# Performance work log

Hardware: AMD Instinct MI355X
Metric: run time of the kernel (lower is better)

The kernel has to match this reference:

```python
import jax, jax.numpy as jnp
import numpy as np

B, S, D = 2, 2048, 2048
H, KVH, HD = 32, 8, 64
ROPE_THETA = 500000.0


def _rope_cos_sin(seq_len, head_dim, theta, batch):
    inv_freq = 1.0 / (theta ** (jnp.arange(0, head_dim, 2, dtype=jnp.float32) / head_dim))  # [HD/2]
    pos = jnp.arange(seq_len, dtype=jnp.float32)
    freqs = jnp.outer(pos, inv_freq)                      # [S, HD/2]
    emb = jnp.concatenate([freqs, freqs], axis=-1)        # [S, HD]
    cos = jnp.broadcast_to(jnp.cos(emb), (batch, seq_len, head_dim))
    sin = jnp.broadcast_to(jnp.sin(emb), (batch, seq_len, head_dim))
    return cos, sin


def setup_inputs() -> dict:
    key = jax.random.key(0)
    kx, kq, kk, kv, ko = jax.random.split(key, 5)
    x = jax.random.normal(kx, (B, S, D), dtype=jnp.float32)
    cos, sin = _rope_cos_sin(S, HD, ROPE_THETA, B)
    scale = 0.02
    Wq = jax.random.normal(kq, (H * HD, D), dtype=jnp.float32) * scale
    Wk = jax.random.normal(kk, (KVH * HD, D), dtype=jnp.float32) * scale
    Wv = jax.random.normal(kv, (KVH * HD, D), dtype=jnp.float32) * scale
    Wo = jax.random.normal(ko, (D, H * HD), dtype=jnp.float32) * scale
    return {"x": x, "cos": cos, "sin": sin, "Wq": Wq, "Wk": Wk, "Wv": Wv, "Wo": Wo}


def rotate_half(t):
    t1, t2 = jnp.split(t, 2, axis=-1)
    return jnp.concatenate([-t2, t1], axis=-1)


def reference(x, cos, sin, Wq, Wk, Wv, Wo):
    b, s, d = x.shape
    scaling = HD ** -0.5
    groups = H // KVH
    # projections (torch Linear: y = x @ W.T)
    q = jnp.einsum('bsd,od->bso', x, Wq).reshape(b, s, H, HD).transpose(0, 2, 1, 3)    # [B,H,S,HD]
    k = jnp.einsum('bsd,od->bso', x, Wk).reshape(b, s, KVH, HD).transpose(0, 2, 1, 3)  # [B,KVH,S,HD]
    v = jnp.einsum('bsd,od->bso', x, Wv).reshape(b, s, KVH, HD).transpose(0, 2, 1, 3)
    # RoPE (cos/sin unsqueezed over head dim)
    c = cos[:, None, :, :]
    sn = sin[:, None, :, :]
    q = q * c + rotate_half(q) * sn
    k = k * c + rotate_half(k) * sn
    # GQA: repeat kv heads
    k = jnp.repeat(k, groups, axis=1)  # [B,H,S,HD]
    v = jnp.repeat(v, groups, axis=1)
    # causal eager SDPA
    scores = jnp.einsum('bhqd,bhkd->bhqk', q, k) * scaling
    causal = jnp.tril(jnp.ones((s, s), dtype=bool))
    scores = jnp.where(causal[None, None], scores, jnp.finfo(scores.dtype).min)
    attn_weights = jax.nn.softmax(scores, axis=-1)
    attn = jnp.einsum('bhqk,bhkd->bhqd', attn_weights, v)
    attn = attn.transpose(0, 2, 1, 3).reshape(b, s, H * HD)
    out = jnp.einsum('bso,do->bsd', attn, Wo)
    return out
```

## Files before the change

### kernel.cpp

```cpp
#include <hip/hip_runtime.h>
#include <hip/hip_bf16.h>

typedef __attribute__((ext_vector_type(8))) short bf16x8_t;
typedef __attribute__((ext_vector_type(4))) float f32x4;

#define S_LEN  2048
#define NB     2
#define NH     32
#define NKVH   8
#define HD     64
#define DMODEL 2048
#define SCALE  0.125f
#define CEXP   0.18033688f
#define THRRAW 44.0f

__device__ __forceinline__ void gload16(const __hip_bfloat16* g, __hip_bfloat16* l) {
  __builtin_amdgcn_global_load_lds(
      (const __attribute__((address_space(1))) void*)g,
      (__attribute__((address_space(3))) void*)l, 16, 0, 0);
}

struct CvtSeg { const float* src; __hip_bfloat16* dst; int n4; };
struct CvtArgs { CvtSeg s[5]; };

__global__ __launch_bounds__(256) void cvt_all(CvtArgs a) {
  int i = blockIdx.x * blockDim.x + threadIdx.x;
#pragma unroll
  for (int k = 0; k < 5; ++k) {
    if (i < a.s[k].n4) {
      float4 v = ((const float4*)a.s[k].src)[i];
      __hip_bfloat16 o0 = __float2bfloat16(v.x), o1 = __float2bfloat16(v.y);
      __hip_bfloat16 o2 = __float2bfloat16(v.z), o3 = __float2bfloat16(v.w);
      ushort4 pk;
      pk.x = *(unsigned short*)&o0; pk.y = *(unsigned short*)&o1;
      pk.z = *(unsigned short*)&o2; pk.w = *(unsigned short*)&o3;
      ((ushort4*)a.s[k].dst)[i] = pk;
      return;
    }
    i -= a.s[k].n4;
  }
}

__global__ __launch_bounds__(256)
void gemm_qkv(const __hip_bfloat16* __restrict__ A,
              const __hip_bfloat16* __restrict__ Wq,
              const __hip_bfloat16* __restrict__ Wk,
              const __hip_bfloat16* __restrict__ Wv,
              __hip_bfloat16* __restrict__ Qo,
              __hip_bfloat16* __restrict__ Ko,
              __hip_bfloat16* __restrict__ Vto,
              const float* __restrict__ cosb,
              const float* __restrict__ sinb)
{
  __shared__ __align__(16) __hip_bfloat16 As[2][128][32];
  __shared__ __align__(16) __hip_bfloat16 Bs[2][128][32];
  const int K = DMODEL;

  const int tid  = threadIdx.x;
  const int lane = tid & 63;
  const int w    = tid >> 6;
  const int wr   = (w >> 1) * 64;
  const int wc   = (w & 1) * 64;
  const int brow = blockIdx.y * 128;
  const int fr   = lane & 15;
  const int fg   = lane >> 4;

  const int bc = blockIdx.x * 128;
  const __hip_bfloat16* Bt; int bcol; int path;
  if (bc < 2048)      { Bt = Wq; bcol = bc;        path = 0; }
  else if (bc < 2560) { Bt = Wk; bcol = bc - 2048; path = 1; }
  else                { Bt = Wv; bcol = bc - 2560; path = 2; }

  const f32x4 fz = {0.f, 0.f, 0.f, 0.f};
  f32x4 acc[4][4];
#pragma unroll
  for (int i = 0; i < 4; ++i)
#pragma unroll
    for (int j = 0; j < 4; ++j) acc[i][j] = fz;

  const int lrow = lane >> 2;
  const int lcol = (lane & 3) * 8;
  const __hip_bfloat16* Ag = A  + (size_t)(brow + w * 32 + lrow) * K + lcol;
  const __hip_bfloat16* Bg = Bt + (size_t)(bcol + w * 32 + lrow) * K + lcol;

  auto stage = [&](int buf, int kt) {
    gload16(Ag + kt,                    &As[buf][w * 32][0]);
    gload16(Ag + (size_t)16 * K + kt,   &As[buf][w * 32 + 16][0]);
    gload16(Bg + kt,                    &Bs[buf][w * 32][0]);
    gload16(Bg + (size_t)16 * K + kt,   &Bs[buf][w * 32 + 16][0]);
  };

  stage(0, 0);
  __syncthreads();
  int cur = 0;
  for (int kt = 0; kt < K; kt += 32) {
    if (kt + 32 < K) stage(cur ^ 1, kt + 32);

    bf16x8_t af[4], bfr[4];
#pragma unroll
    for (int mi = 0; mi < 4; ++mi)
      af[mi] = *(const bf16x8_t*)&As[cur][wr + mi * 16 + fr][fg * 8];
#pragma unroll
    for (int ni = 0; ni < 4; ++ni)
      bfr[ni] = *(const bf16x8_t*)&Bs[cur][wc + ni * 16 + fr][fg * 8];
#pragma unroll
    for (int mi = 0; mi < 4; ++mi)
#pragma unroll
      for (int ni = 0; ni < 4; ++ni)
        acc[mi][ni] = __builtin_amdgcn_mfma_f32_16x16x32_bf16(af[mi], bfr[ni], acc[mi][ni], 0, 0, 0);

    __syncthreads();
    cur ^= 1;
  }

  if (path == 2) {
#pragma unroll
    for (int mi = 0; mi < 4; ++mi) {
#pragma unroll
      for (int ni = 0; ni < 4; ++ni) {
        const int row0 = brow + wr + mi * 16 + fg * 4;
        const int col  = bcol + wc + ni * 16 + fr;
        const int b = row0 >> 11, s = row0 & 2047;
        const int kvh = col >> 6, d = col & 63;
        __hip_bfloat16 v0 = __float2bfloat16(acc[mi][ni][0]);
        __hip_bfloat16 v1 = __float2bfloat16(acc[mi][ni][1]);
        __hip_bfloat16 v2 = __float2bfloat16(acc[mi][ni][2]);
        __hip_bfloat16 v3 = __float2bfloat16(acc[mi][ni][3]);
        ushort4 pk;
        pk.x = *(unsigned short*)&v0; pk.y = *(unsigned short*)&v1;
        pk.z = *(unsigned short*)&v2; pk.w = *(unsigned short*)&v3;
        *(ushort4*)&Vto[(((size_t)b * NKVH + kvh) * HD + d) * S_LEN + s] = pk;
      }
    }
  } else {
    __hip_bfloat16* C = (path == 0) ? Qo : Ko;
    const int N = (path == 0) ? (NH * HD) : (NKVH * HD);
#pragma unroll
    for (int mi = 0; mi < 4; ++mi) {
#pragma unroll
      for (int r = 0; r < 4; ++r) {
        const int row = brow + wr + mi * 16 + fg * 4 + r;
#pragma unroll
        for (int ni = 0; ni < 2; ++ni) {
          const int colL = bcol + wc + ni * 16 + fr;
          const int d    = (colL & 63);
          const float c  = cosb[(size_t)row * HD + d];
          const float sn = sinb[(size_t)row * HD + d];
          const float v0 = acc[mi][ni][r];
          const float v1 = acc[mi][ni + 2][r];
          C[(size_t)row * N + colL]      = __float2bfloat16(v0 * c - v1 * sn);
          C[(size_t)row * N + colL + 32] = __float2bfloat16(v1 * c + v0 * sn);
        }
      }
    }
  }
}

__global__ __launch_bounds__(256)
void gemm_o(const __hip_bfloat16* __restrict__ A,
            const __hip_bfloat16* __restrict__ Bt,
            float* __restrict__ C)
{
  __shared__ __align__(16) __hip_bfloat16 As[2][128][32];
  __shared__ __align__(16) __hip_bfloat16 Bs[2][128][32];
  const int K = DMODEL, N = DMODEL;

  const int tid  = threadIdx.x;
  const int lane = tid & 63;
  const int w    = tid >> 6;
  const int wr   = (w >> 1) * 64;
  const int wc   = (w & 1) * 64;
  const int brow = blockIdx.y * 128;
  const int bcol = blockIdx.x * 128;
  const int fr   = lane & 15;
  const int fg   = lane >> 4;

  const f32x4 fz = {0.f, 0.f, 0.f, 0.f};
  f32x4 acc[4][4];
#pragma unroll
  for (int i = 0; i < 4; ++i)
#pragma unroll
    for (int j = 0; j < 4; ++j) acc[i][j] = fz;

  const int lrow = lane >> 2;
  const int lcol = (lane & 3) * 8;
  const __hip_bfloat16* Ag = A  + (size_t)(brow + w * 32 + lrow) * K + lcol;
  const __hip_bfloat16* Bg = Bt + (size_t)(bcol + w * 32 + lrow) * K + lcol;

  auto stage = [&](int buf, int kt) {
    gload16(Ag + kt,                  &As[buf][w * 32][0]);
    gload16(Ag + (size_t)16 * K + kt, &As[buf][w * 32 + 16][0]);
    gload16(Bg + kt,                  &Bs[buf][w * 32][0]);
    gload16(Bg + (size_t)16 * K + kt, &Bs[buf][w * 32 + 16][0]);
  };

  stage(0, 0);
  __syncthreads();
  int cur = 0;
  for (int kt = 0; kt < K; kt += 32) {
    if (kt + 32 < K) stage(cur ^ 1, kt + 32);

    bf16x8_t af[4], bfr[4];
#pragma unroll
    for (int mi = 0; mi < 4; ++mi)
      af[mi] = *(const bf16x8_t*)&As[cur][wr + mi * 16 + fr][fg * 8];
#pragma unroll
    for (int ni = 0; ni < 4; ++ni)
      bfr[ni] = *(const bf16x8_t*)&Bs[cur][wc + ni * 16 + fr][fg * 8];
#pragma unroll
    for (int mi = 0; mi < 4; ++mi)
#pragma unroll
      for (int ni = 0; ni < 4; ++ni)
        acc[mi][ni] = __builtin_amdgcn_mfma_f32_16x16x32_bf16(af[mi], bfr[ni], acc[mi][ni], 0, 0, 0);

    __syncthreads();
    cur ^= 1;
  }

#pragma unroll
  for (int mi = 0; mi < 4; ++mi)
#pragma unroll
    for (int ni = 0; ni < 4; ++ni) {
      const int row0 = brow + wr + mi * 16 + fg * 4;
      const int col  = bcol + wc + ni * 16 + fr;
#pragma unroll
      for (int r = 0; r < 4; ++r)
        C[(size_t)(row0 + r) * N + col] = acc[mi][ni][r];
    }
}

__global__ __launch_bounds__(512, 6)
void attn_kernel(const __hip_bfloat16* __restrict__ Q, const __hip_bfloat16* __restrict__ K,
                 const __hip_bfloat16* __restrict__ Vt, __hip_bfloat16* __restrict__ O)
{
  __shared__ __align__(16) __hip_bfloat16 Ks[2][64][64];
  __shared__ __align__(16) __hip_bfloat16 Vs[2][64][64];
  __shared__ __align__(16) __hip_bfloat16 Ps[8][16][72];

  const int lane = threadIdx.x & 63;
  const int w    = threadIdx.x >> 6;
  const int fr   = lane & 15;
  const int fg   = lane >> 4;
  const int r8   = lane >> 3;
  const int j8   = lane & 7;
  const int bh   = blockIdx.y;
  const int b    = bh >> 5;
  const int h    = bh & 31;
  const int kvh  = h >> 2;
  const int qt    = gridDim.x - 1 - blockIdx.x;
  const int qbase = qt * 128;
  const int base_s = qbase + w * 16;

  const __hip_bfloat16* Qg = Q + ((size_t)(b * S_LEN + qbase)) * DMODEL + h * HD;
  const __hip_bfloat16* Kg = K + (size_t)b * S_LEN * (NKVH * HD) + kvh * HD;
  const __hip_bfloat16* Vg = Vt + ((size_t)(b * NKVH + kvh)) * HD * S_LEN;

  bf16x8_t qf[2];
#pragma unroll
  for (int kk = 0; kk < 2; ++kk)
    qf[kk] = *(const bf16x8_t*)(Qg + (size_t)(w * 16 + fr) * DMODEL + kk * 32 + fg * 8);

  const f32x4 fz = {0.f, 0.f, 0.f, 0.f};
  f32x4 acc[4];
#pragma unroll
  for (int i = 0; i < 4; ++i) acc[i] = fz;
  float m_ = -1e30f;
  float l_ = 0.f;

  auto stage = [&](int buf, int kt) {
    const int rb = (w & 3) * 16;
    if (w < 4) {
      gload16(Kg + (size_t)(kt + rb + r8)     * (NKVH * HD) + (j8 ^ r8) * 8, &Ks[buf][rb][0]);
      gload16(Kg + (size_t)(kt + rb + 8 + r8) * (NKVH * HD) + (j8 ^ r8) * 8, &Ks[buf][rb + 8][0]);
    } else {
      gload16(Vg + (size_t)(rb + r8)     * S_LEN + kt + (j8 ^ r8) * 8, &Vs[buf][rb][0]);
      gload16(Vg + (size_t)(rb + 8 + r8) * S_LEN + kt + (j8 ^ r8) * 8, &Vs[buf][rb + 8][0]);
    }
  };
  auto ldK = [&](int buf, int row, int cidx) -> bf16x8_t {
    return *(const bf16x8_t*)&Ks[buf][row][(cidx ^ (row & 7)) * 8];
  };
  auto ldV = [&](int buf, int row, int cidx) -> bf16x8_t {
    return *(const bf16x8_t*)&Vs[buf][row][(cidx ^ (row & 7)) * 8];
  };

  stage(0, 0);
  __syncthreads();
  int cur = 0;
  const int NT = 2 * qt + 2;
  for (int t = 0; t < NT; ++t) {
    const int kt = t * 64;
    if (t + 1 < NT) stage(cur ^ 1, kt + 64);

    if (kt <= base_s + 15) {
      f32x4 sc[4];
#pragma unroll
      for (int c = 0; c < 4; ++c) {
        const int krow = c * 16 + fr;
        bf16x8_t k0 = ldK(cur, krow, fg);
        bf16x8_t k1 = ldK(cur, krow, 4 + fg);
        sc[c] = __builtin_amdgcn_mfma_f32_16x16x32_bf16(k0, qf[0], fz, 0, 0, 0);
        sc[c] = __builtin_amdgcn_mfma_f32_16x16x32_bf16(k1, qf[1], sc[c], 0, 0, 0);
      }

      float p[4][4];
      float tm = -3.0e38f;
      if (kt + 63 > base_s) {
#pragma unroll
        for (int c = 0; c < 4; ++c)
#pragma unroll
          for (int r = 0; r < 4; ++r) {
            float v = sc[c][r];
            if (kt + c * 16 + fg * 4 + r > base_s + fr) v = -3.0e38f;
            p[c][r] = v; tm = fmaxf(tm, v);
          }
      } else {
#pragma unroll
        for (int c = 0; c < 4; ++c)
#pragma unroll
          for (int r = 0; r < 4; ++r) { p[c][r] = sc[c][r]; tm = fmaxf(tm, sc[c][r]); }
      }
      tm = fmaxf(tm, __shfl_xor(tm, 16));
      tm = fmaxf(tm, __shfl_xor(tm, 32));

      if (!__all(tm <= m_ + THRRAW)) {
        const float mnew = fmaxf(m_, tm);
        const float sf = exp2f((m_ - mnew) * CEXP);
        m_ = mnew;
        l_ *= sf;
        float sfv[4];
#pragma unroll
        for (int r = 0; r < 4; ++r) sfv[r] = __shfl(sf, fg * 4 + r);
#pragma unroll
        for (int fc = 0; fc < 4; ++fc)
#pragma unroll
          for (int r = 0; r < 4; ++r) acc[fc][r] *= sfv[r];
      }

      float ts = 0.f;
#pragma unroll
      for (int c = 0; c < 4; ++c)
#pragma unroll
        for (int r = 0; r < 4; ++r) {
          p[c][r] = exp2f((p[c][r] - m_) * CEXP);
          ts += p[c][r];
        }
      l_ += ts;

#pragma unroll
      for (int c = 0; c < 4; ++c) {
        __hip_bfloat16 b0 = __float2bfloat16(p[c][0]);
        __hip_bfloat16 b1 = __float2bfloat16(p[c][1]);
        __hip_bfloat16 b2 = __float2bfloat16(p[c][2]);
        __hip_bfloat16 b3 = __float2bfloat16(p[c][3]);
        ushort4 pk;
        pk.x = *(unsigned short*)&b0; pk.y = *(unsigned short*)&b1;
        pk.z = *(unsigned short*)&b2; pk.w = *(unsigned short*)&b3;
        *(ushort4*)&Ps[w][fr][c * 16 + fg * 4] = pk;
      }

#pragma unroll
      for (int kk = 0; kk < 2; ++kk) {
        bf16x8_t pa = *(const bf16x8_t*)&Ps[w][fr][kk * 32 + fg * 8];
#pragma unroll
        for (int fc = 0; fc < 4; ++fc) {
          bf16x8_t vf = ldV(cur, fc * 16 + fr, kk * 4 + fg);
          acc[fc] = __builtin_amdgcn_mfma_f32_16x16x32_bf16(pa, vf, acc[fc], 0, 0, 0);
        }
      }
    }

    __syncthreads();
    cur ^= 1;
  }

  l_ += __shfl_xor(l_, 16);
  l_ += __shfl_xor(l_, 32);
  float lv[4];
#pragma unroll
  for (int r = 0; r < 4; ++r) lv[r] = __builtin_amdgcn_rcpf(__shfl(l_, fg * 4 + r));
#pragma unroll
  for (int fc = 0; fc < 4; ++fc)
#pragma unroll
    for (int r = 0; r < 4; ++r) {
      const size_t row = (size_t)(b * S_LEN + base_s + fg * 4 + r);
      O[row * DMODEL + h * HD + fc * 16 + fr] = __float2bfloat16(acc[fc][r] * lv[r]);
    }
}

extern "C" void kernel_launch(void* const* d_in, const int* in_sizes, int n_in,
                              void* d_out, int out_size, void* d_ws, size_t ws_size,
                              hipStream_t stream)
{
  const float* x    = (const float*)d_in[0];
  const float* cosb = (const float*)d_in[1];
  const float* sinb = (const float*)d_in[2];
  const float* Wq   = (const float*)d_in[3];
  const float* Wk   = (const float*)d_in[4];
  const float* Wv   = (const float*)d_in[5];
  const float* Wo   = (const float*)d_in[6];
  float* out = (float*)d_out;

  char* p = (char*)d_ws;
  __hip_bfloat16* x_bf    = (__hip_bfloat16*)p; p += (size_t)NB * S_LEN * DMODEL * 2;
  __hip_bfloat16* Wq_bf   = (__hip_bfloat16*)p; p += (size_t)NH * HD * DMODEL * 2;
  __hip_bfloat16* Wk_bf   = (__hip_bfloat16*)p; p += (size_t)NKVH * HD * DMODEL * 2;
  __hip_bfloat16* Wv_bf   = (__hip_bfloat16*)p; p += (size_t)NKVH * HD * DMODEL * 2;
  __hip_bfloat16* Wo_bf   = (__hip_bfloat16*)p; p += (size_t)DMODEL * NH * HD * 2;
  __hip_bfloat16* Q_bf    = (__hip_bfloat16*)p; p += (size_t)NB * S_LEN * NH * HD * 2;
  __hip_bfloat16* K_bf    = (__hip_bfloat16*)p; p += (size_t)NB * S_LEN * NKVH * HD * 2;
  __hip_bfloat16* Vt_bf   = (__hip_bfloat16*)p; p += (size_t)NB * NKVH * HD * S_LEN * 2;
  __hip_bfloat16* attn_bf = (__hip_bfloat16*)p; p += (size_t)NB * S_LEN * NH * HD * 2;

  CvtArgs ca;
  ca.s[0] = { x,  x_bf,  (int)((size_t)NB * S_LEN * DMODEL / 4) };
  ca.s[1] = { Wq, Wq_bf, (int)((size_t)NH * HD * DMODEL / 4) };
  ca.s[2] = { Wk, Wk_bf, (int)((size_t)NKVH * HD * DMODEL / 4) };
  ca.s[3] = { Wv, Wv_bf, (int)((size_t)NKVH * HD * DMODEL / 4) };
  ca.s[4] = { Wo, Wo_bf, (int)((size_t)DMODEL * NH * HD / 4) };
  int total4 = ca.s[0].n4 + ca.s[1].n4 + ca.s[2].n4 + ca.s[3].n4 + ca.s[4].n4;
  cvt_all<<<(total4 + 255) / 256, 256, 0, stream>>>(ca);

  gemm_qkv<<<dim3(3072 / 128, (NB * S_LEN) / 128), dim3(256), 0, stream>>>(
      x_bf, Wq_bf, Wk_bf, Wv_bf, Q_bf, K_bf, Vt_bf, cosb, sinb);

  attn_kernel<<<dim3(S_LEN / 128, NB * NH), dim3(512), 0, stream>>>(Q_bf, K_bf, Vt_bf, attn_bf);

  gemm_o<<<dim3(DMODEL / 128, (NB * S_LEN) / 128), dim3(256), 0, stream>>>(attn_bf, Wo_bf, out);
}
```

Before: 377.3 us.

## Load attention K/V directly from global per wave and swizzle blocks across XCDs

The attention kernel drops the shared-memory double-buffered K/V staging and block-wide barriers. Each wave now loads its K and V fragments straight from global memory into registers and runs only the key tiles its causal range needs. All three kernels also remap block IDs so neighbouring tiles are spread across the XCDs, aiming for better L2 reuse. The attention occupancy hint drops from 6 to 4 because of the extra registers. This removes LDS traffic and syncs, but the eight waves of a block now each reload the same K/V tiles from global memory/L2, and there is no software prefetch.

```diff
diff --git a/kernel.cpp b/kernel.cpp
--- a/kernel.cpp
+++ b/kernel.cpp
@@ -18,6 +18,10 @@
   __builtin_amdgcn_global_load_lds(
       (const __attribute__((address_space(1))) void*)g,
       (__attribute__((address_space(3))) void*)l, 16, 0, 0);
+}
+
+__device__ __forceinline__ int xcd_swz(int bid, int nwg) {
+  return (bid & 7) * (nwg >> 3) + (bid >> 3);
 }
 
 struct CvtSeg { const float* src; __hip_bfloat16* dst; int n4; };
@@ -61,11 +65,16 @@
   const int w    = tid >> 6;
   const int wr   = (w >> 1) * 64;
   const int wc   = (w & 1) * 64;
-  const int brow = blockIdx.y * 128;
   const int fr   = lane & 15;
   const int fg   = lane >> 4;
 
-  const int bc = blockIdx.x * 128;
+  const int nwg = gridDim.x * gridDim.y;
+  const int swz = xcd_swz(blockIdx.y * gridDim.x + blockIdx.x, nwg);
+  const int bx  = swz % gridDim.x;
+  const int by  = swz / gridDim.x;
+  const int brow = by * 128;
+
+  const int bc = bx * 128;
   const __hip_bfloat16* Bt; int bcol; int path;
   if (bc < 2048)      { Bt = Wq; bcol = bc;        path = 0; }
   else if (bc < 2560) { Bt = Wk; bcol = bc - 2048; path = 1; }
@@ -170,10 +179,15 @@
   const int w    = tid >> 6;
   const int wr   = (w >> 1) * 64;
   const int wc   = (w & 1) * 64;
-  const int brow = blockIdx.y * 128;
-  const int bcol = blockIdx.x * 128;
   const int fr   = lane & 15;
   const int fg   = lane >> 4;
+
+  const int nwg = gridDim.x * gridDim.y;
+  const int swz = xcd_swz(blockIdx.y * gridDim.x + blockIdx.x, nwg);
+  const int bx  = swz % gridDim.x;
+  const int by  = swz / gridDim.x;
+  const int brow = by * 128;
+  const int bcol = bx * 128;
 
   const f32x4 fz = {0.f, 0.f, 0.f, 0.f};
   f32x4 acc[4][4];
@@ -229,30 +243,31 @@
     }
 }
 
-__global__ __launch_bounds__(512, 6)
+__global__ __launch_bounds__(512, 4)
 void attn_kernel(const __hip_bfloat16* __restrict__ Q, const __hip_bfloat16* __restrict__ K,
                  const __hip_bfloat16* __restrict__ Vt, __hip_bfloat16* __restrict__ O)
 {
-  __shared__ __align__(16) __hip_bfloat16 Ks[2][64][64];
-  __shared__ __align__(16) __hip_bfloat16 Vs[2][64][64];
   __shared__ __align__(16) __hip_bfloat16 Ps[8][16][72];
 
   const int lane = threadIdx.x & 63;
   const int w    = threadIdx.x >> 6;
   const int fr   = lane & 15;
   const int fg   = lane >> 4;
-  const int r8   = lane >> 3;
-  const int j8   = lane & 7;
-  const int bh   = blockIdx.y;
+
+  const int nwg = gridDim.x * gridDim.y;
+  const int swz = xcd_swz(blockIdx.y * gridDim.x + blockIdx.x, nwg);
+  const int bx  = swz & 15;
+  const int bh  = swz >> 4;
   const int b    = bh >> 5;
   const int h    = bh & 31;
   const int kvh  = h >> 2;
-  const int qt    = gridDim.x - 1 - blockIdx.x;
-  const int qbase = qt * 128;
+  const int qt     = 15 - bx;
+  const int qbase  = qt * 128;
   const int base_s = qbase + w * 16;
+  const int KSTR   = NKVH * HD;
 
   const __hip_bfloat16* Qg = Q + ((size_t)(b * S_LEN + qbase)) * DMODEL + h * HD;
-  const __hip_bfloat16* Kg = K + (size_t)b * S_LEN * (NKVH * HD) + kvh * HD;
+  const __hip_bfloat16* Kg = K + (size_t)b * S_LEN * KSTR + kvh * HD;
   const __hip_bfloat16* Vg = Vt + ((size_t)(b * NKVH + kvh)) * HD * S_LEN;
 
   bf16x8_t qf[2];
@@ -267,111 +282,98 @@
   float m_ = -1e30f;
   float l_ = 0.f;
 
-  auto stage = [&](int buf, int kt) {
-    const int rb = (w & 3) * 16;
-    if (w < 4) {
-      gload16(Kg + (size_t)(kt + rb + r8)     * (NKVH * HD) + (j8 ^ r8) * 8, &Ks[buf][rb][0]);
-      gload16(Kg + (size_t)(kt + rb + 8 + r8) * (NKVH * HD) + (j8 ^ r8) * 8, &Ks[buf][rb + 8][0]);
+  const int NTw = ((base_s + 15) >> 6) + 1;
+  for (int t = 0; t < NTw; ++t) {
+    const int kt = t * 64;
+
+    const __hip_bfloat16* Kt = Kg + (size_t)(kt + fr) * KSTR + fg * 8;
+    bf16x8_t k0[4], k1[4];
+#pragma unroll
+    for (int c = 0; c < 4; ++c) {
+      k0[c] = *(const bf16x8_t*)(Kt + (size_t)(c * 16) * KSTR);
+      k1[c] = *(const bf16x8_t*)(Kt + (size_t)(c * 16) * KSTR + 32);
+    }
+
+    f32x4 sc[4];
+#pragma unroll
+    for (int c = 0; c < 4; ++c) {
+      sc[c] = __builtin_amdgcn_mfma_f32_16x16x32_bf16(k0[c], qf[0], fz, 0, 0, 0);
+      sc[c] = __builtin_amdgcn_mfma_f32_16x16x32_bf16(k1[c], qf[1], sc[c], 0, 0, 0);
+    }
+
+    const __hip_bfloat16* Vp = Vg + (size_t)fr * S_LEN + kt + fg * 8;
+    bf16x8_t v0[4], v1[4];
+#pragma unroll
+    for (int fc = 0; fc < 4; ++fc) {
+      v0[fc] = *(const bf16x8_t*)(Vp + (size_t)(fc * 16) * S_LEN);
+      v1[fc] = *(const bf16x8_t*)(Vp + (size_t)(fc * 16) * S_LEN + 32);
+    }
+
+    float p[4][4];
+    float tm = -3.0e38f;
+    if (kt + 63 > base_s) {
+#pragma unroll
+      for (int c = 0; c < 4; ++c)
+#pragma unroll
+        for (int r = 0; r < 4; ++r) {
+          float v = sc[c][r];
+          if (kt + c * 16 + fg * 4 + r > base_s + fr) v = -3.0e38f;
+          p[c][r] = v; tm = fmaxf(tm, v);
+        }
     } else {
-      gload16(Vg + (size_t)(rb + r8)     * S_LEN + kt + (j8 ^ r8) * 8, &Vs[buf][rb][0]);
-      gload16(Vg + (size_t)(rb + 8 + r8) * S_LEN + kt + (j8 ^ r8) * 8, &Vs[buf][rb + 8][0]);
-    }
-  };
-  auto ldK = [&](int buf, int row, int cidx) -> bf16x8_t {
-    return *(const bf16x8_t*)&Ks[buf][row][(cidx ^ (row & 7)) * 8];
-  };
-  auto ldV = [&](int buf, int row, int cidx) -> bf16x8_t {
-    return *(const bf16x8_t*)&Vs[buf][row][(cidx ^ (row & 7)) * 8];
-  };
-
-  stage(0, 0);
-  __syncthreads();
-  int cur = 0;
-  const int NT = 2 * qt + 2;
-  for (int t = 0; t < NT; ++t) {
-    const int kt = t * 64;
-    if (t + 1 < NT) stage(cur ^ 1, kt + 64);
-
-    if (kt <= base_s + 15) {
-      f32x4 sc[4];
-#pragma unroll
-      for (int c = 0; c < 4; ++c) {
-        const int krow = c * 16 + fr;
-        bf16x8_t k0 = ldK(cur, krow, fg);
-        bf16x8_t k1 = ldK(cur, krow, 4 + fg);
-        sc[c] = __builtin_amdgcn_mfma_f32_16x16x32_bf16(k0, qf[0], fz, 0, 0, 0);
-        sc[c] = __builtin_amdgcn_mfma_f32_16x16x32_bf16(k1, qf[1], sc[c], 0, 0, 0);
+#pragma unroll
+      for (int c = 0; c < 4; ++c)
+#pragma unroll
+        for (int r = 0; r < 4; ++r) { p[c][r] = sc[c][r]; tm = fmaxf(tm, sc[c][r]); }
+    }
+    tm = fmaxf(tm, __shfl_xor(tm, 16));
+    tm = fmaxf(tm, __shfl_xor(tm, 32));
+
+    if (!__all(tm <= m_ + THRRAW)) {
+      const float mnew = fmaxf(m_, tm);
+      const float sf = exp2f((m_ - mnew) * CEXP);
+      m_ = mnew;
+      l_ *= sf;
+      float sfv[4];
+#pragma unroll
+      for (int r = 0; r < 4; ++r) sfv[r] = __shfl(sf, fg * 4 + r);
+#pragma unroll
+      for (int fc = 0; fc < 4; ++fc)
+#pragma unroll
+        for (int r = 0; r < 4; ++r) acc[fc][r] *= sfv[r];
+    }
+
+    float ts = 0.f;
+#pragma unroll
+    for (int c = 0; c < 4; ++c)
+#pragma unroll
+      for (int r = 0; r < 4; ++r) {
+        p[c][r] = exp2f((p[c][r] - m_) * CEXP);
+        ts += p[c][r];
       }
-
-      float p[4][4];
-      float tm = -3.0e38f;
-      if (kt + 63 > base_s) {
-#pragma unroll
-        for (int c = 0; c < 4; ++c)
-#pragma unroll
-          for (int r = 0; r < 4; ++r) {
-            float v = sc[c][r];
-            if (kt + c * 16 + fg * 4 + r > base_s + fr) v = -3.0e38f;
-            p[c][r] = v; tm = fmaxf(tm, v);
-          }
-      } else {
-#pragma unroll
-        for (int c = 0; c < 4; ++c)
-#pragma unroll
-          for (int r = 0; r < 4; ++r) { p[c][r] = sc[c][r]; tm = fmaxf(tm, sc[c][r]); }
+    l_ += ts;
+
+#pragma unroll
+    for (int c = 0; c < 4; ++c) {
+      __hip_bfloat16 b0 = __float2bfloat16(p[c][0]);
+      __hip_bfloat16 b1 = __float2bfloat16(p[c][1]);
+      __hip_bfloat16 b2 = __float2bfloat16(p[c][2]);
+      __hip_bfloat16 b3 = __float2bfloat16(p[c][3]);
+      ushort4 pk;
+      pk.x = *(unsigned short*)&b0; pk.y = *(unsigned short*)&b1;
+      pk.z = *(unsigned short*)&b2; pk.w = *(unsigned short*)&b3;
+      *(ushort4*)&Ps[w][fr][c * 16 + fg * 4] = pk;
+    }
+
+#pragma unroll
+    for (int kk = 0; kk < 2; ++kk) {
+      bf16x8_t pa = *(const bf16x8_t*)&Ps[w][fr][kk * 32 + fg * 8];
+#pragma unroll
+      for (int fc = 0; fc < 4; ++fc) {
+        bf16x8_t vf = (kk == 0) ? v0[fc] : v1[fc];
+        acc[fc] = __builtin_amdgcn_mfma_f32_16x16x32_bf16(pa, vf, acc[fc], 0, 0, 0);
       }
-      tm = fmaxf(tm, __shfl_xor(tm, 16));
-      tm = fmaxf(tm, __shfl_xor(tm, 32));
-
-      if (!__all(tm <= m_ + THRRAW)) {
-        const float mnew = fmaxf(m_, tm);
-        const float sf = exp2f((m_ - mnew) * CEXP);
-        m_ = mnew;
-        l_ *= sf;
-        float sfv[4];
-#pragma unroll
-        for (int r = 0; r < 4; ++r) sfv[r] = __shfl(sf, fg * 4 + r);
-#pragma unroll
-        for (int fc = 0; fc < 4; ++fc)
-#pragma unroll
-          for (int r = 0; r < 4; ++r) acc[fc][r] *= sfv[r];
-      }
-
-      float ts = 0.f;
-#pragma unroll
-      for (int c = 0; c < 4; ++c)
-#pragma unroll
-        for (int r = 0; r < 4; ++r) {
-          p[c][r] = exp2f((p[c][r] - m_) * CEXP);
-          ts += p[c][r];
-        }
-      l_ += ts;
-
-#pragma unroll
-      for (int c = 0; c < 4; ++c) {
-        __hip_bfloat16 b0 = __float2bfloat16(p[c][0]);
-        __hip_bfloat16 b1 = __float2bfloat16(p[c][1]);
-        __hip_bfloat16 b2 = __float2bfloat16(p[c][2]);
-        __hip_bfloat16 b3 = __float2bfloat16(p[c][3]);
-        ushort4 pk;
-        pk.x = *(unsigned short*)&b0; pk.y = *(unsigned short*)&b1;
-        pk.z = *(unsigned short*)&b2; pk.w = *(unsigned short*)&b3;
-        *(ushort4*)&Ps[w][fr][c * 16 + fg * 4] = pk;
-      }
-
-#pragma unroll
-      for (int kk = 0; kk < 2; ++kk) {
-        bf16x8_t pa = *(const bf16x8_t*)&Ps[w][fr][kk * 32 + fg * 8];
-#pragma unroll
-        for (int fc = 0; fc < 4; ++fc) {
-          bf16x8_t vf = ldV(cur, fc * 16 + fr, kk * 4 + fg);
-          acc[fc] = __builtin_amdgcn_mfma_f32_16x16x32_bf16(pa, vf, acc[fc], 0, 0, 0);
-        }
-      }
-    }
-
-    __syncthreads();
-    cur ^= 1;
+    }
   }
 
   l_ += __shfl_xor(l_, 16);
```

Result: slower. 607.4 us (+61.0%).

## Double attention Q tile per block and add XCD-aware block swizzle to GEMMs

Applied to the files above, without the earlier changes.

The attention kernel now gives each wave two 16-row query subtiles, so a block covers 256 query rows. Every K/V tile staged in LDS therefore serves twice as many queries, which halves K/V global traffic and the number of blocks. The cost is more accumulator registers, so launch bounds drop occupancy from 6 to 4, and the coarser causal tiles give less load balance across blocks. Both GEMMs also remap block IDs with an XCD swizzle so that neighbouring tiles share L2.

```diff
diff --git a/kernel.cpp b/kernel.cpp
--- a/kernel.cpp
+++ b/kernel.cpp
@@ -18,6 +18,10 @@
   __builtin_amdgcn_global_load_lds(
       (const __attribute__((address_space(1))) void*)g,
       (__attribute__((address_space(3))) void*)l, 16, 0, 0);
+}
+
+__device__ __forceinline__ int xcd_swz(int bid, int nwg) {
+  return (bid & 7) * (nwg >> 3) + (bid >> 3);
 }
 
 struct CvtSeg { const float* src; __hip_bfloat16* dst; int n4; };
@@ -61,11 +65,16 @@
   const int w    = tid >> 6;
   const int wr   = (w >> 1) * 64;
   const int wc   = (w & 1) * 64;
-  const int brow = blockIdx.y * 128;
   const int fr   = lane & 15;
   const int fg   = lane >> 4;
 
-  const int bc = blockIdx.x * 128;
+  const int nwg = gridDim.x * gridDim.y;
+  const int swz = xcd_swz(blockIdx.y * gridDim.x + blockIdx.x, nwg);
+  const int bx  = swz % gridDim.x;
+  const int by  = swz / gridDim.x;
+  const int brow = by * 128;
+
+  const int bc = bx * 128;
   const __hip_bfloat16* Bt; int bcol; int path;
   if (bc < 2048)      { Bt = Wq; bcol = bc;        path = 0; }
   else if (bc < 2560) { Bt = Wk; bcol = bc - 2048; path = 1; }
@@ -170,10 +179,15 @@
   const int w    = tid >> 6;
   const int wr   = (w >> 1) * 64;
   const int wc   = (w & 1) * 64;
-  const int brow = blockIdx.y * 128;
-  const int bcol = blockIdx.x * 128;
   const int fr   = lane & 15;
   const int fg   = lane >> 4;
+
+  const int nwg = gridDim.x * gridDim.y;
+  const int swz = xcd_swz(blockIdx.y * gridDim.x + blockIdx.x, nwg);
+  const int bx  = swz % gridDim.x;
+  const int by  = swz / gridDim.x;
+  const int brow = by * 128;
+  const int bcol = bx * 128;
 
   const f32x4 fz = {0.f, 0.f, 0.f, 0.f};
   f32x4 acc[4][4];
@@ -229,7 +243,7 @@
     }
 }
 
-__global__ __launch_bounds__(512, 6)
+__global__ __launch_bounds__(512, 4)
 void attn_kernel(const __hip_bfloat16* __restrict__ Q, const __hip_bfloat16* __restrict__ K,
                  const __hip_bfloat16* __restrict__ Vt, __hip_bfloat16* __restrict__ O)
 {
@@ -248,24 +262,28 @@
   const int h    = bh & 31;
   const int kvh  = h >> 2;
   const int qt    = gridDim.x - 1 - blockIdx.x;
-  const int qbase = qt * 128;
-  const int base_s = qbase + w * 16;
+  const int qbase = qt * 256;
+  const int wbase = qbase + w * 32;
 
   const __hip_bfloat16* Qg = Q + ((size_t)(b * S_LEN + qbase)) * DMODEL + h * HD;
   const __hip_bfloat16* Kg = K + (size_t)b * S_LEN * (NKVH * HD) + kvh * HD;
   const __hip_bfloat16* Vg = Vt + ((size_t)(b * NKVH + kvh)) * HD * S_LEN;
 
-  bf16x8_t qf[2];
-#pragma unroll
-  for (int kk = 0; kk < 2; ++kk)
-    qf[kk] = *(const bf16x8_t*)(Qg + (size_t)(w * 16 + fr) * DMODEL + kk * 32 + fg * 8);
+  bf16x8_t qf[2][2];
+#pragma unroll
+  for (int s = 0; s < 2; ++s)
+#pragma unroll
+    for (int kk = 0; kk < 2; ++kk)
+      qf[s][kk] = *(const bf16x8_t*)(Qg + (size_t)(w * 32 + s * 16 + fr) * DMODEL + kk * 32 + fg * 8);
 
   const f32x4 fz = {0.f, 0.f, 0.f, 0.f};
-  f32x4 acc[4];
-#pragma unroll
-  for (int i = 0; i < 4; ++i) acc[i] = fz;
-  float m_ = -1e30f;
-  float l_ = 0.f;
+  f32x4 acc[2][4];
+#pragma unroll
+  for (int s = 0; s < 2; ++s)
+#pragma unroll
+    for (int i = 0; i < 4; ++i) acc[s][i] = fz;
+  float m_[2] = {-1e30f, -1e30f};
+  float l_[2] = {0.f, 0.f};
 
   auto stage = [&](int buf, int kt) {
     const int rb = (w & 3) * 16;
@@ -287,85 +305,90 @@
   stage(0, 0);
   __syncthreads();
   int cur = 0;
-  const int NT = 2 * qt + 2;
+  const int NT = 4 * qt + 4;
   for (int t = 0; t < NT; ++t) {
     const int kt = t * 64;
     if (t + 1 < NT) stage(cur ^ 1, kt + 64);
 
-    if (kt <= base_s + 15) {
-      f32x4 sc[4];
-#pragma unroll
-      for (int c = 0; c < 4; ++c) {
-        const int krow = c * 16 + fr;
-        bf16x8_t k0 = ldK(cur, krow, fg);
-        bf16x8_t k1 = ldK(cur, krow, 4 + fg);
-        sc[c] = __builtin_amdgcn_mfma_f32_16x16x32_bf16(k0, qf[0], fz, 0, 0, 0);
-        sc[c] = __builtin_amdgcn_mfma_f32_16x16x32_bf16(k1, qf[1], sc[c], 0, 0, 0);
-      }
-
-      float p[4][4];
-      float tm = -3.0e38f;
-      if (kt + 63 > base_s) {
+    if (kt <= wbase) {
+#pragma unroll
+      for (int s = 0; s < 2; ++s) {
+        const int base_s = wbase + s * 16;
+
+        f32x4 sc[4];
+#pragma unroll
+        for (int c = 0; c < 4; ++c) {
+          const int krow = c * 16 + fr;
+          bf16x8_t k0 = ldK(cur, krow, fg);
+          bf16x8_t k1 = ldK(cur, krow, 4 + fg);
+          sc[c] = __builtin_amdgcn_mfma_f32_16x16x32_bf16(k0, qf[s][0], fz, 0, 0, 0);
+          sc[c] = __builtin_amdgcn_mfma_f32_16x16x32_bf16(k1, qf[s][1], sc[c], 0, 0, 0);
+        }
+
+        float p[4][4];
+        float tm = -3.0e38f;
+        if (kt + 63 > base_s) {
+#pragma unroll
+          for (int c = 0; c < 4; ++c)
+#pragma unroll
+            for (int r = 0; r < 4; ++r) {
+              float v = sc[c][r];
+              if (kt + c * 16 + fg * 4 + r > base_s + fr) v = -3.0e38f;
+              p[c][r] = v; tm = fmaxf(tm, v);
+            }
+        } else {
+#pragma unroll
+          for (int c = 0; c < 4; ++c)
+#pragma unroll
+            for (int r = 0; r < 4; ++r) { p[c][r] = sc[c][r]; tm = fmaxf(tm, sc[c][r]); }
+        }
+        tm = fmaxf(tm, __shfl_xor(tm, 16));
+        tm = fmaxf(tm, __shfl_xor(tm, 32));
+
+        if (!__all(tm <= m_[s] + THRRAW)) {
+          const float mnew = fmaxf(m_[s], tm);
+          const float sf = exp2f((m_[s] - mnew) * CEXP);
+          m_[s] = mnew;
+          l_[s] *= sf;
+          float sfv[4];
+#pragma unroll
+          for (int r = 0; r < 4; ++r) sfv[r] = __shfl(sf, fg * 4 + r);
+#pragma unroll
+          for (int fc = 0; fc < 4; ++fc)
+#pragma unroll
+            for (int r = 0; r < 4; ++r) acc[s][fc][r] *= sfv[r];
+        }
+
+        float ts = 0.f;
 #pragma unroll
         for (int c = 0; c < 4; ++c)
 #pragma unroll
           for (int r = 0; r < 4; ++r) {
-            float v = sc[c][r];
-            if (kt + c * 16 + fg * 4 + r > base_s + fr) v = -3.0e38f;
-            p[c][r] = v; tm = fmaxf(tm, v);
+            p[c][r] = exp2f((p[c][r] - m_[s]) * CEXP);
+            ts += p[c][r];
           }
-      } else {
-#pragma unroll
-        for (int c = 0; c < 4; ++c)
-#pragma unroll
-          for (int r = 0; r < 4; ++r) { p[c][r] = sc[c][r]; tm = fmaxf(tm, sc[c][r]); }
-      }
-      tm = fmaxf(tm, __shfl_xor(tm, 16));
-      tm = fmaxf(tm, __shfl_xor(tm, 32));
-
-      if (!__all(tm <= m_ + THRRAW)) {
-        const float mnew = fmaxf(m_, tm);
-        const float sf = exp2f((m_ - mnew) * CEXP);
-        m_ = mnew;
-        l_ *= sf;
-        float sfv[4];
-#pragma unroll
-        for (int r = 0; r < 4; ++r) sfv[r] = __shfl(sf, fg * 4 + r);
-#pragma unroll
-        for (int fc = 0; fc < 4; ++fc)
-#pragma unroll
-          for (int r = 0; r < 4; ++r) acc[fc][r] *= sfv[r];
-      }
-
-      float ts = 0.f;
-#pragma unroll
-      for (int c = 0; c < 4; ++c)
-#pragma unroll
-        for (int r = 0; r < 4; ++r) {
-          p[c][r] = exp2f((p[c][r] - m_) * CEXP);
-          ts += p[c][r];
-        }
-      l_ += ts;
-
-#pragma unroll
-      for (int c = 0; c < 4; ++c) {
-        __hip_bfloat16 b0 = __float2bfloat16(p[c][0]);
-        __hip_bfloat16 b1 = __float2bfloat16(p[c][1]);
-        __hip_bfloat16 b2 = __float2bfloat16(p[c][2]);
-        __hip_bfloat16 b3 = __float2bfloat16(p[c][3]);
-        ushort4 pk;
-        pk.x = *(unsigned short*)&b0; pk.y = *(unsigned short*)&b1;
-        pk.z = *(unsigned short*)&b2; pk.w = *(unsigned short*)&b3;
-        *(ushort4*)&Ps[w][fr][c * 16 + fg * 4] = pk;
-      }
-
-#pragma unroll
-      for (int kk = 0; kk < 2; ++kk) {
-        bf16x8_t pa = *(const bf16x8_t*)&Ps[w][fr][kk * 32 + fg * 8];
-#pragma unroll
-        for (int fc = 0; fc < 4; ++fc) {
-          bf16x8_t vf = ldV(cur, fc * 16 + fr, kk * 4 + fg);
-          acc[fc] = __builtin_amdgcn_mfma_f32_16x16x32_bf16(pa, vf, acc[fc], 0, 0, 0);
+        l_[s] += ts;
+
+#pragma unroll
+        for (int c = 0; c < 4; ++c) {
+          __hip_bfloat16 b0 = __float2bfloat16(p[c][0]);
+          __hip_bfloat16 b1 = __float2bfloat16(p[c][1]);
+          __hip_bfloat16 b2 = __float2bfloat16(p[c][2]);
+          __hip_bfloat16 b3 = __float2bfloat16(p[c][3]);
+          ushort4 pk;
+          pk.x = *(unsigned short*)&b0; pk.y = *(unsigned short*)&b1;
+          pk.z = *(unsigned short*)&b2; pk.w = *(unsigned short*)&b3;
+          *(ushort4*)&Ps[w][fr][c * 16 + fg * 4] = pk;
+        }
+
+#pragma unroll
+        for (int kk = 0; kk < 2; ++kk) {
+          bf16x8_t pa = *(const bf16x8_t*)&Ps[w][fr][kk * 32 + fg * 8];
+#pragma unroll
+          for (int fc = 0; fc < 4; ++fc) {
+            bf16x8_t vf = ldV(cur, fc * 16 + fr, kk * 4 + fg);
+            acc[s][fc] = __builtin_amdgcn_mfma_f32_16x16x32_bf16(pa, vf, acc[s][fc], 0, 0, 0);
+          }
         }
       }
     }
@@ -374,18 +397,22 @@
     cur ^= 1;
   }
 
-  l_ += __shfl_xor(l_, 16);
-  l_ += __shfl_xor(l_, 32);
-  float lv[4];
-#pragma unroll
-  for (int r = 0; r < 4; ++r) lv[r] = __builtin_amdgcn_rcpf(__shfl(l_, fg * 4 + r));
-#pragma unroll
-  for (int fc = 0; fc < 4; ++fc)
-#pragma unroll
-    for (int r = 0; r < 4; ++r) {
-      const size_t row = (size_t)(b * S_LEN + base_s + fg * 4 + r);
-      O[row * DMODEL + h * HD + fc * 16 + fr] = __float2bfloat16(acc[fc][r] * lv[r]);
-    }
+#pragma unroll
+  for (int s = 0; s < 2; ++s) {
+    float l = l_[s];
+    l += __shfl_xor(l, 16);
+    l += __shfl_xor(l, 32);
+    float lv[4];
+#pragma unroll
+    for (int r = 0; r < 4; ++r) lv[r] = __builtin_amdgcn_rcpf(__shfl(l, fg * 4 + r));
+#pragma unroll
+    for (int fc = 0; fc < 4; ++fc)
+#pragma unroll
+      for (int r = 0; r < 4; ++r) {
+        const size_t row = (size_t)(b * S_LEN + wbase + s * 16 + fg * 4 + r);
+        O[row * DMODEL + h * HD + fc * 16 + fr] = __float2bfloat16(acc[s][fc][r] * lv[r]);
+      }
+  }
 }
 
 extern "C" void kernel_launch(void* const* d_in, const int* in_sizes, int n_in,
@@ -424,7 +451,7 @@
   gemm_qkv<<<dim3(3072 / 128, (NB * S_LEN) / 128), dim3(256), 0, stream>>>(
       x_bf, Wq_bf, Wk_bf, Wv_bf, Q_bf, K_bf, Vt_bf, cosb, sinb);
 
-  attn_kernel<<<dim3(S_LEN / 128, NB * NH), dim3(512), 0, stream>>>(Q_bf, K_bf, Vt_bf, attn_bf);
+  attn_kernel<<<dim3(S_LEN / 256, NB * NH), dim3(512), 0, stream>>>(Q_bf, K_bf, Vt_bf, attn_bf);
 
   gemm_o<<<dim3(DMODEL / 128, (NB * S_LEN) / 128), dim3(256), 0, stream>>>(attn_bf, Wo_bf, out);
 }
```

Measured after the change: 388.3 us. +2.9%, slower.
